# Kernel optimization log

Hardware: AMD Instinct MI355X
Metric: run time of the kernel (lower is better)

## Reference

```python
import jax, jax.numpy as jnp
import numpy as np


def setup_inputs() -> dict:
    key = jax.random.key(0)
    ks = jax.random.split(key, 8)
    B, C, H, W = 4, 256, 64, 64
    Cqk = C // 8
    s = 1.0 / np.sqrt(C)
    return {
        "x": jax.random.normal(ks[0], (B, C, H, W), jnp.float32),
        "wq": jax.random.normal(ks[1], (Cqk, C), jnp.float32) * s,
        "bq": jax.random.normal(ks[2], (Cqk,), jnp.float32) * 0.01,
        "wk": jax.random.normal(ks[3], (Cqk, C), jnp.float32) * s,
        "bk": jax.random.normal(ks[4], (Cqk,), jnp.float32) * 0.01,
        "wv": jax.random.normal(ks[5], (C, C), jnp.float32) * s,
        "bv": jax.random.normal(ks[6], (C,), jnp.float32) * 0.01,
        "gamma": jax.random.normal(ks[7], (1,), jnp.float32),
    }


def reference(x, wq, bq, wk, bk, wv, bv, gamma):
    B, C, H, W = x.shape
    N = H * W
    xf = x.reshape(B, C, N)  # [B, C, N]
    # 1x1 convs are per-pixel channel matmuls
    q = jnp.einsum('oc,bcn->bon', wq, xf) + bq[None, :, None]  # [B, C//8, N]
    k = jnp.einsum('oc,bcn->bon', wk, xf) + bk[None, :, None]  # [B, C//8, N]
    v = jnp.einsum('oc,bcn->bon', wv, xf) + bv[None, :, None]  # [B, C, N]
    # energy[b, n, m] = q[b,:,n] . k[b,:,m]  (unscaled)
    energy = jnp.einsum('bcn,bcm->bnm', q, k)  # [B, N, N]
    # original applies softmax over dim=-2, i.e. over the query index n per column m
    attn = jax.nn.softmax(energy, axis=-2)  # [B, N, N]
    at_map = jnp.transpose(attn, (0, 2, 1))  # returned map, [B, N, N]
    # sa_map = V @ attn : bmm([B,C,N],[B,N,N]) -> [B,C,N]
    sa = jnp.einsum('bcn,bnm->bcm', v, attn).reshape(B, C, H, W)
    out = x + gamma[0] * sa
    return (out, at_map)
```

## Files before the change

### kernel.cpp

```cpp
#include <hip/hip_runtime.h>
#include <hip/hip_bf16.h>
#include <cstdint>
#include <cstddef>

#define NPIX 4096
#define CIN  256
#define CQK  32
#define BSZ  4

typedef __attribute__((ext_vector_type(8))) short          bf16x8;
typedef __attribute__((ext_vector_type(4))) float          f32x4;
typedef __attribute__((ext_vector_type(8))) unsigned short u16x8;

static __device__ inline unsigned short f2bf(float f) {
    __hip_bfloat16 h = __float2bfloat16(f);
    unsigned short u;
    __builtin_memcpy(&u, &h, 2);
    return u;
}

static __device__ inline void gl2lds16(const void* g, void* l) {
    __builtin_amdgcn_global_load_lds(
        (const __attribute__((address_space(1))) unsigned int*)g,
        (__attribute__((address_space(3))) unsigned int*)l,
        16, 0, 0);
}

__global__ __launch_bounds__(256) void proj_kernel(
    const float* __restrict__ x, const float* __restrict__ W,
    const float* __restrict__ bias, float* __restrict__ y, int Cout)
{
    __shared__ float Wl[8][CIN];
    const int t  = threadIdx.x;
    const int n0 = blockIdx.x * 1024;
    const int o0 = blockIdx.y * 8;
    const int b  = blockIdx.z;

    #pragma unroll
    for (int j = 0; j < 8; ++j) {
        int flat = t + 256 * j;
        int row = flat >> 8, col = flat & 255;
        Wl[row][col] = W[(o0 + row) * CIN + col];
    }
    __syncthreads();

    float acc[8][4];
    #pragma unroll
    for (int o = 0; o < 8; ++o)
        #pragma unroll
        for (int i = 0; i < 4; ++i) acc[o][i] = 0.f;

    const float* xb = x + ((size_t)b * CIN) * NPIX + n0 + t * 4;
    #pragma unroll 4
    for (int c = 0; c < CIN; ++c) {
        float4 xv = *(const float4*)(xb + (size_t)c * NPIX);
        #pragma unroll
        for (int o = 0; o < 8; ++o) {
            float w = Wl[o][c];
            acc[o][0] = fmaf(w, xv.x, acc[o][0]);
            acc[o][1] = fmaf(w, xv.y, acc[o][1]);
            acc[o][2] = fmaf(w, xv.z, acc[o][2]);
            acc[o][3] = fmaf(w, xv.w, acc[o][3]);
        }
    }
    #pragma unroll
    for (int o = 0; o < 8; ++o) {
        float bb = bias[o0 + o];
        float4 r = { acc[o][0] + bb, acc[o][1] + bb,
                     acc[o][2] + bb, acc[o][3] + bb };
        *(float4*)(y + ((size_t)(b * Cout + o0 + o)) * NPIX + n0 + t * 4) = r;
    }
}

__global__ __launch_bounds__(256) void proj_qk_kernel(
    const float* __restrict__ x,
    const float* __restrict__ wq, const float* __restrict__ bq,
    const float* __restrict__ wk, const float* __restrict__ bk,
    float* __restrict__ qout, float* __restrict__ kout)
{
    __shared__ float Wl[CIN][12];
    const int t  = threadIdx.x;
    const int n0 = blockIdx.x * 512;
    const int og = blockIdx.y * 8;
    const int b  = blockIdx.z;
    const bool isK = og >= CQK;
    const float* W    = isK ? wk : wq;
    const float* bias = isK ? bk : bq;
    float* y          = isK ? kout : qout;
    const int o0      = isK ? og - CQK : og;

    #pragma unroll
    for (int j = 0; j < 8; ++j) {
        int flat = t + 256 * j;
        int o = flat >> 8, c = flat & 255;
        Wl[c][o] = W[(o0 + o) * CIN + c];
    }
    __syncthreads();

    float acc[8][2];
    #pragma unroll
    for (int o = 0; o < 8; ++o) { acc[o][0] = 0.f; acc[o][1] = 0.f; }

    const float* xb = x + ((size_t)b * CIN) * NPIX + n0 + t * 2;
    #pragma unroll 4
    for (int c = 0; c < CIN; ++c) {
        float2 xv = *(const float2*)(xb + (size_t)c * NPIX);
        f32x4 w0 = *(const f32x4*)&Wl[c][0];
        f32x4 w1 = *(const f32x4*)&Wl[c][4];
        float wv[8] = { w0[0], w0[1], w0[2], w0[3],
                        w1[0], w1[1], w1[2], w1[3] };
        #pragma unroll
        for (int o = 0; o < 8; ++o) {
            acc[o][0] = fmaf(wv[o], xv.x, acc[o][0]);
            acc[o][1] = fmaf(wv[o], xv.y, acc[o][1]);
        }
    }
    #pragma unroll
    for (int o = 0; o < 8; ++o) {
        float bb = bias[o0 + o];
        float2 r = { acc[o][0] + bb, acc[o][1] + bb };
        *(float2*)(y + ((size_t)(b * CQK + o0 + o)) * NPIX + n0 + t * 2) = r;
    }
}

__global__ __launch_bounds__(256) void proj_v_bf16_kernel(
    const float* __restrict__ x, const float* __restrict__ W,
    const float* __restrict__ bias, unsigned short* __restrict__ y)
{
    __shared__ float Wl[CIN][20];
    const int t  = threadIdx.x;
    const int n0 = blockIdx.x * 512;
    const int o0 = blockIdx.y * 16;
    const int b  = blockIdx.z;

    #pragma unroll
    for (int j = 0; j < 16; ++j) {
        int flat = t + 256 * j;
        int o = flat >> 8, c = flat & 255;
        Wl[c][o] = W[(o0 + o) * CIN + c];
    }
    __syncthreads();

    float acc[16][2];
    #pragma unroll
    for (int o = 0; o < 16; ++o) { acc[o][0] = 0.f; acc[o][1] = 0.f; }

    const float* xb = x + ((size_t)b * CIN) * NPIX + n0 + t * 2;
    #pragma unroll 2
    for (int c = 0; c < CIN; ++c) {
        float2 xv = *(const float2*)(xb + (size_t)c * NPIX);
        f32x4 w0 = *(const f32x4*)&Wl[c][0];
        f32x4 w1 = *(const f32x4*)&Wl[c][4];
        f32x4 w2 = *(const f32x4*)&Wl[c][8];
        f32x4 w3 = *(const f32x4*)&Wl[c][12];
        float wv[16] = { w0[0], w0[1], w0[2], w0[3],
                         w1[0], w1[1], w1[2], w1[3],
                         w2[0], w2[1], w2[2], w2[3],
                         w3[0], w3[1], w3[2], w3[3] };
        #pragma unroll
        for (int o = 0; o < 16; ++o) {
            acc[o][0] = fmaf(wv[o], xv.x, acc[o][0]);
            acc[o][1] = fmaf(wv[o], xv.y, acc[o][1]);
        }
    }
    #pragma unroll
    for (int o = 0; o < 16; ++o) {
        float bb = bias[o0 + o];
        ushort2 r;
        r.x = f2bf(acc[o][0] + bb);
        r.y = f2bf(acc[o][1] + bb);
        *(ushort2*)(y + ((size_t)(b * CIN + o0 + o)) * NPIX + n0 + t * 2) = r;
    }
}

__global__ __launch_bounds__(512) void energy_softmax_kernel(
    const float* __restrict__ q, const float* __restrict__ k,
    float* __restrict__ at_map, unsigned short* __restrict__ attn_bf,
    float* __restrict__ inv_buf)
{
    __shared__ float kk[CQK][12];
    __shared__ float wredM[8][8];
    __shared__ float wredS[8][8];
    const int t  = threadIdx.x;
    const int m0 = blockIdx.x * 8;
    const int b  = blockIdx.y;
    const int lane = t & 63, wid = t >> 6;

    if (t < 256) {
        int c = t >> 3, mi = t & 7;
        kk[c][mi] = k[((size_t)(b * CQK + c)) * NPIX + m0 + mi];
    }
    __syncthreads();

    float s[8][8];
    #pragma unroll
    for (int mi = 0; mi < 8; ++mi)
        #pragma unroll
        for (int i = 0; i < 8; ++i) s[mi][i] = 0.f;

    const float* qb = q + ((size_t)b * CQK) * NPIX + t * 8;
    #pragma unroll 2
    for (int c = 0; c < CQK; ++c) {
        float4 q0 = *(const float4*)(qb + (size_t)c * NPIX);
        float4 q1 = *(const float4*)(qb + (size_t)c * NPIX + 4);
        f32x4 k0 = *(const f32x4*)&kk[c][0];
        f32x4 k1 = *(const f32x4*)&kk[c][4];
        float kv[8] = { k0[0], k0[1], k0[2], k0[3],
                        k1[0], k1[1], k1[2], k1[3] };
        #pragma unroll
        for (int mi = 0; mi < 8; ++mi) {
            float w = kv[mi];
            s[mi][0] = fmaf(w, q0.x, s[mi][0]);
            s[mi][1] = fmaf(w, q0.y, s[mi][1]);
            s[mi][2] = fmaf(w, q0.z, s[mi][2]);
            s[mi][3] = fmaf(w, q0.w, s[mi][3]);
            s[mi][4] = fmaf(w, q1.x, s[mi][4]);
            s[mi][5] = fmaf(w, q1.y, s[mi][5]);
            s[mi][6] = fmaf(w, q1.z, s[mi][6]);
            s[mi][7] = fmaf(w, q1.w, s[mi][7]);
        }
    }

    #pragma unroll
    for (int mi = 0; mi < 8; ++mi) {
        float mx = s[mi][0];
        #pragma unroll
        for (int i = 1; i < 8; ++i) mx = fmaxf(mx, s[mi][i]);
        #pragma unroll
        for (int off = 1; off < 64; off <<= 1)
            mx = fmaxf(mx, __shfl_xor(mx, off, 64));
        if (lane == 0) wredM[mi][wid] = mx;
    }
    __syncthreads();

    #pragma unroll
    for (int mi = 0; mi < 8; ++mi) {
        float bmx = wredM[mi][0];
        #pragma unroll
        for (int w = 1; w < 8; ++w) bmx = fmaxf(bmx, wredM[mi][w]);
        float sum = 0.f;
        #pragma unroll
        for (int i = 0; i < 8; ++i) {
            s[mi][i] = __expf(s[mi][i] - bmx);
            sum += s[mi][i];
        }
        if (attn_bf) {
            size_t rowoff = ((size_t)(b * NPIX) + m0 + mi) * NPIX + t * 8;
            u16x8 rb;
            #pragma unroll
            for (int i = 0; i < 8; ++i) rb[i] = f2bf(s[mi][i]);
            *(u16x8*)(attn_bf + rowoff) = rb;
        }
        #pragma unroll
        for (int off = 1; off < 64; off <<= 1)
            sum += __shfl_xor(sum, off, 64);
        if (lane == 0) wredS[mi][wid] = sum;
    }
    __syncthreads();

    #pragma unroll
    for (int mi = 0; mi < 8; ++mi) {
        float bsum = 0.f;
        #pragma unroll
        for (int w = 0; w < 8; ++w) bsum += wredS[mi][w];
        float inv = 1.f / bsum;
        if (inv_buf && t == mi) inv_buf[(size_t)b * NPIX + m0 + mi] = inv;
        size_t rowoff = ((size_t)(b * NPIX) + m0 + mi) * NPIX + t * 8;
        float4 r0 = { s[mi][0]*inv, s[mi][1]*inv, s[mi][2]*inv, s[mi][3]*inv };
        float4 r1 = { s[mi][4]*inv, s[mi][5]*inv, s[mi][6]*inv, s[mi][7]*inv };
        *(float4*)(at_map + rowoff)     = r0;
        *(float4*)(at_map + rowoff + 4) = r1;
    }
}

__global__ __launch_bounds__(256) void sa_gemm_mfma(
    const unsigned short* __restrict__ v,
    const unsigned short* __restrict__ attn,
    const float* __restrict__ x, const float* __restrict__ gptr,
    const float* __restrict__ inv_buf,
    float* __restrict__ out)
{
    __shared__ __align__(16) unsigned short As[128 * 64];
    __shared__ __align__(16) unsigned short Bs[64 * 64];

    const int t = threadIdx.x, lane = t & 63, w = t >> 6;

    const int gid  = blockIdx.x;
    const int xcd  = gid & 7;
    const int slot = gid >> 3;
    const int c_t     = slot & 1;
    const int m_local = (slot >> 1) & 7;
    const int b       = slot >> 4;
    const int m_base = (xcd * 8 + m_local) * 64;
    const int c_base = c_t * 128;
    const int wc = (w >> 1) * 64, wm = (w & 1) * 32;

    const int lrow = lane >> 3;
    const int glog = (lane & 7) ^ lrow;
    const unsigned short* aSrc[4];
    const unsigned short* bSrc[2];
    #pragma unroll
    for (int qi = 0; qi < 4; ++qi)
        aSrc[qi] = v    + ((size_t)(b * CIN + c_base + w * 32 + qi * 8 + lrow)) * NPIX + glog * 8;
    #pragma unroll
    for (int qi = 0; qi < 2; ++qi)
        bSrc[qi] = attn + ((size_t)b * NPIX + m_base + w * 16 + qi * 8 + lrow) * NPIX + glog * 8;

    const int l15 = lane & 15, q4 = lane >> 4;
    const int x0 = (q4 ^ (lane & 7)) * 8;
    const int x1 = ((q4 ^ 4) ^ (lane & 7)) * 8;
    const int baseA = (wc + l15) * 64;
    const int baseB = (wm + l15) * 64;

    f32x4 acc[4][2];
    #pragma unroll
    for (int i = 0; i < 4; ++i)
        #pragma unroll
        for (int j = 0; j < 2; ++j) acc[i][j] = (f32x4)(0.0f);

    for (int k0 = 0; k0 < NPIX; k0 += 64) {
        #pragma unroll
        for (int qi = 0; qi < 4; ++qi)
            gl2lds16(aSrc[qi] + k0, &As[(w * 32 + qi * 8) * 64]);
        #pragma unroll
        for (int qi = 0; qi < 2; ++qi)
            gl2lds16(bSrc[qi] + k0, &Bs[(w * 16 + qi * 8) * 64]);
        __syncthreads();
        #pragma unroll
        for (int ks = 0; ks < 2; ++ks) {
            const int xo = ks ? x1 : x0;
            bf16x8 af[4], bfr[2];
            #pragma unroll
            for (int i = 0; i < 4; ++i)
                af[i] = *(const bf16x8*)&As[baseA + i * 1024 + xo];
            #pragma unroll
            for (int j = 0; j < 2; ++j)
                bfr[j] = *(const bf16x8*)&Bs[baseB + j * 1024 + xo];
            #pragma unroll
            for (int i = 0; i < 4; ++i)
                #pragma unroll
                for (int j = 0; j < 2; ++j)
                    acc[i][j] = __builtin_amdgcn_mfma_f32_16x16x32_bf16(
                        af[i], bfr[j], acc[i][j], 0, 0, 0);
        }
        __syncthreads();
    }

    const float g = gptr[0];
    float invm[2];
    #pragma unroll
    for (int j = 0; j < 2; ++j)
        invm[j] = inv_buf[(size_t)b * NPIX + m_base + wm + j * 16 + l15];
    #pragma unroll
    for (int i = 0; i < 4; ++i) {
        int c = c_base + wc + i * 16 + q4 * 4;
        #pragma unroll
        for (int j = 0; j < 2; ++j) {
            int m = m_base + wm + j * 16 + l15;
            float gi = g * invm[j];
            #pragma unroll
            for (int r = 0; r < 4; ++r) {
                size_t idx = ((size_t)(b * CIN + c + r)) * NPIX + m;
                out[idx] = x[idx] + gi * acc[i][j][r];
            }
        }
    }
}

__global__ __launch_bounds__(256) void sa_gemm_kernel(
    const float* __restrict__ v, const float* __restrict__ at_map,
    const float* __restrict__ x, const float* __restrict__ gptr,
    float* __restrict__ out)
{
    __shared__ float Vt[32][68];
    __shared__ float At[32][68];
    const int t  = threadIdx.x;
    const int m0 = blockIdx.x * 64;
    const int c0 = blockIdx.y * 64;
    const int b  = blockIdx.z;
    const int r  = t >> 2, qd = t & 3;
    const int tc = t & 15, tm = t >> 4;

    const float* vb = v      + ((size_t)(b * CIN  + c0 + r)) * NPIX + qd * 4;
    const float* ab = at_map + ((size_t)(b * NPIX + m0 + r)) * NPIX + qd * 4;

    float acc[4][4];
    #pragma unroll
    for (int i = 0; i < 4; ++i)
        #pragma unroll
        for (int j = 0; j < 4; ++j) acc[i][j] = 0.f;

    for (int n0 = 0; n0 < NPIX; n0 += 32) {
        float4 v0 = *(const float4*)(vb + n0);
        float4 v1 = *(const float4*)(vb + n0 + 16);
        float4 a0 = *(const float4*)(ab + n0);
        float4 a1 = *(const float4*)(ab + n0 + 16);
        Vt[qd*4+0][r] = v0.x; Vt[qd*4+1][r] = v0.y;
        Vt[qd*4+2][r] = v0.z; Vt[qd*4+3][r] = v0.w;
        Vt[16+qd*4+0][r] = v1.x; Vt[16+qd*4+1][r] = v1.y;
        Vt[16+qd*4+2][r] = v1.z; Vt[16+qd*4+3][r] = v1.w;
        At[qd*4+0][r] = a0.x; At[qd*4+1][r] = a0.y;
        At[qd*4+2][r] = a0.z; At[qd*4+3][r] = a0.w;
        At[16+qd*4+0][r] = a1.x; At[16+qd*4+1][r] = a1.y;
        At[16+qd*4+2][r] = a1.z; At[16+qd*4+3][r] = a1.w;
        __syncthreads();
        #pragma unroll
        for (int kk = 0; kk < 32; ++kk) {
            float4 a  = *(const float4*)&Vt[kk][tc * 4];
            float4 bb = *(const float4*)&At[kk][tm * 4];
            acc[0][0] = fmaf(a.x, bb.x, acc[0][0]);
            acc[0][1] = fmaf(a.x, bb.y, acc[0][1]);
            acc[0][2] = fmaf(a.x, bb.z, acc[0][2]);
            acc[0][3] = fmaf(a.x, bb.w, acc[0][3]);
            acc[1][0] = fmaf(a.y, bb.x, acc[1][0]);
            acc[1][1] = fmaf(a.y, bb.y, acc[1][1]);
            acc[1][2] = fmaf(a.y, bb.z, acc[1][2]);
            acc[1][3] = fmaf(a.y, bb.w, acc[1][3]);
            acc[2][0] = fmaf(a.z, bb.x, acc[2][0]);
            acc[2][1] = fmaf(a.z, bb.y, acc[2][1]);
            acc[2][2] = fmaf(a.z, bb.z, acc[2][2]);
            acc[2][3] = fmaf(a.z, bb.w, acc[2][3]);
            acc[3][0] = fmaf(a.w, bb.x, acc[3][0]);
            acc[3][1] = fmaf(a.w, bb.y, acc[3][1]);
            acc[3][2] = fmaf(a.w, bb.z, acc[3][2]);
            acc[3][3] = fmaf(a.w, bb.w, acc[3][3]);
        }
        __syncthreads();
    }

    const float g = *gptr;
    #pragma unroll
    for (int i = 0; i < 4; ++i) {
        size_t row = ((size_t)(b * CIN + c0 + tc * 4 + i)) * NPIX + m0 + tm * 4;
        float4 xv = *(const float4*)(x + row);
        float4 o  = { xv.x + g * acc[i][0], xv.y + g * acc[i][1],
                      xv.z + g * acc[i][2], xv.w + g * acc[i][3] };
        *(float4*)(out + row) = o;
    }
}

extern "C" void kernel_launch(void* const* d_in, const int* in_sizes, int n_in,
                              void* d_out, int out_size, void* d_ws, size_t ws_size,
                              hipStream_t stream) {
    const float* x     = (const float*)d_in[0];
    const float* wq    = (const float*)d_in[1];
    const float* bq    = (const float*)d_in[2];
    const float* wk    = (const float*)d_in[3];
    const float* bk    = (const float*)d_in[4];
    const float* wv    = (const float*)d_in[5];
    const float* bv    = (const float*)d_in[6];
    const float* gamma = (const float*)d_in[7];

    float* out    = (float*)d_out;
    float* at_map = out + (size_t)BSZ * CIN * NPIX;

    const size_t qk_elems  = (size_t)BSZ * CQK * NPIX;
    const size_t v_elems   = (size_t)BSZ * CIN * NPIX;
    const size_t nn_elems  = (size_t)BSZ * NPIX * NPIX;
    const size_t inv_elems = (size_t)BSZ * NPIX;

    const size_t need_fast = 2 * qk_elems * 4 + v_elems * 2 + nn_elems * 2
                           + inv_elems * 4;

    if (ws_size >= need_fast) {
        float*          q       = (float*)d_ws;
        float*          k       = q + qk_elems;
        unsigned short* v_bf    = (unsigned short*)(k + qk_elems);
        unsigned short* attn_bf = v_bf + v_elems;
        float*          inv_buf = (float*)(attn_bf + nn_elems);

        proj_qk_kernel<<<dim3(NPIX/512, 8, BSZ), 256, 0, stream>>>(
            x, wq, bq, wk, bk, q, k);
        proj_v_bf16_kernel<<<dim3(NPIX/512, CIN/16, BSZ), 256, 0, stream>>>(
            x, wv, bv, v_bf);

        energy_softmax_kernel<<<dim3(NPIX/8, BSZ), 512, 0, stream>>>(
            q, k, at_map, attn_bf, inv_buf);

        sa_gemm_mfma<<<dim3(512, 1, 1), 256, 0, stream>>>(
            v_bf, attn_bf, x, gamma, inv_buf, out);
    } else {
        float* q = (float*)d_ws;
        float* k = q + qk_elems;
        float* v = k + qk_elems;

        proj_kernel<<<dim3(NPIX/1024, CQK/8, BSZ), 256, 0, stream>>>(x, wq, bq, q, CQK);
        proj_kernel<<<dim3(NPIX/1024, CQK/8, BSZ), 256, 0, stream>>>(x, wk, bk, k, CQK);
        proj_kernel<<<dim3(NPIX/1024, CIN/8, BSZ), 256, 0, stream>>>(x, wv, bv, v, CIN);

        energy_softmax_kernel<<<dim3(NPIX/8, BSZ), 512, 0, stream>>>(
            q, k, at_map, nullptr, nullptr);

        sa_gemm_kernel<<<dim3(NPIX/64, CIN/64, BSZ), 256, 0, stream>>>(
            v, at_map, x, gamma, out);
    }
}
```

Baseline: 539.7 us.

## Fuse energy, softmax and attention-value GEMM into one two-pass flash-style kernel

Replaces the separate energy/softmax kernel and the bf16 attention GEMM with a single kernel. Each block makes two passes over the keys: the first computes column-wise online max and sum, the second recomputes energies, writes the normalized fp32 attention map and feeds bf16 probabilities through LDS into MFMA against V. This drops the bf16 NxN intermediate buffer write and read and one kernel launch. In exchange it recomputes the QK dot products twice, and each block now covers all 256 channels, which changes occupancy and LDS usage.

Result: no change. 544.4 us (+0.9%).

```diff
diff --git a/kernel.cpp b/kernel.cpp
--- a/kernel.cpp
+++ b/kernel.cpp
@@ -7,6 +7,8 @@
 #define CIN  256
 #define CQK  32
 #define BSZ  4
+#define MT   32
+#define NT   64
 
 typedef __attribute__((ext_vector_type(8))) short          bf16x8;
 typedef __attribute__((ext_vector_type(4))) float          f32x4;
@@ -175,8 +177,7 @@
 
 __global__ __launch_bounds__(512) void energy_softmax_kernel(
     const float* __restrict__ q, const float* __restrict__ k,
-    float* __restrict__ at_map, unsigned short* __restrict__ attn_bf,
-    float* __restrict__ inv_buf)
+    float* __restrict__ at_map)
 {
     __shared__ float kk[CQK][12];
     __shared__ float wredM[8][8];
@@ -244,13 +245,6 @@
             s[mi][i] = __expf(s[mi][i] - bmx);
             sum += s[mi][i];
         }
-        if (attn_bf) {
-            size_t rowoff = ((size_t)(b * NPIX) + m0 + mi) * NPIX + t * 8;
-            u16x8 rb;
-            #pragma unroll
-            for (int i = 0; i < 8; ++i) rb[i] = f2bf(s[mi][i]);
-            *(u16x8*)(attn_bf + rowoff) = rb;
-        }
         #pragma unroll
         for (int off = 1; off < 64; off <<= 1)
             sum += __shfl_xor(sum, off, 64);
@@ -264,7 +258,6 @@
         #pragma unroll
         for (int w = 0; w < 8; ++w) bsum += wredS[mi][w];
         float inv = 1.f / bsum;
-        if (inv_buf && t == mi) inv_buf[(size_t)b * NPIX + m0 + mi] = inv;
         size_t rowoff = ((size_t)(b * NPIX) + m0 + mi) * NPIX + t * 8;
         float4 r0 = { s[mi][0]*inv, s[mi][1]*inv, s[mi][2]*inv, s[mi][3]*inv };
         float4 r1 = { s[mi][4]*inv, s[mi][5]*inv, s[mi][6]*inv, s[mi][7]*inv };
@@ -273,44 +266,114 @@
     }
 }
 
-__global__ __launch_bounds__(256) void sa_gemm_mfma(
+__global__ __launch_bounds__(256) void fused_attn_kernel(
+    const float* __restrict__ q,
+    const float* __restrict__ k,
     const unsigned short* __restrict__ v,
-    const unsigned short* __restrict__ attn,
     const float* __restrict__ x, const float* __restrict__ gptr,
-    const float* __restrict__ inv_buf,
-    float* __restrict__ out)
+    float* __restrict__ at_map, float* __restrict__ out)
 {
-    __shared__ __align__(16) unsigned short As[128 * 64];
-    __shared__ __align__(16) unsigned short Bs[64 * 64];
+    __shared__ __align__(16) unsigned short Vs[CIN * NT];
+    __shared__ __align__(16) float          Qs[2][CQK * NT];
+    __shared__ __align__(16) unsigned short Ps[MT * 72];
+    __shared__ float Ks[CQK][MT];
+    __shared__ float MaxS[MT], InvS[MT];
 
     const int t = threadIdx.x, lane = t & 63, w = t >> 6;
 
-    const int gid  = blockIdx.x;
-    const int xcd  = gid & 7;
-    const int slot = gid >> 3;
-    const int c_t     = slot & 1;
-    const int m_local = (slot >> 1) & 7;
-    const int b       = slot >> 4;
-    const int m_base = (xcd * 8 + m_local) * 64;
-    const int c_base = c_t * 128;
-    const int wc = (w >> 1) * 64, wm = (w & 1) * 32;
-
+    const int gid = blockIdx.x;
+    const int xcd = gid & 7, slot = gid >> 3;
+    const int b = xcd & 3;
+    const int m0 = (slot + ((xcd >> 2) << 6)) * MT;
+
+    const int nq = lane & 15;
+    const int mp = w * 4 + (lane >> 4);
+    const int mA = 2 * mp, mB = 2 * mp + 1;
+    const int l15 = lane & 15, q4 = lane >> 4;
+    const int wc = w * 64;
+    const int xo0 = (q4 ^ (l15 & 7)) * 8;
+    const int xo1 = ((q4 ^ 4) ^ (l15 & 7)) * 8;
     const int lrow = lane >> 3;
     const int glog = (lane & 7) ^ lrow;
-    const unsigned short* aSrc[4];
-    const unsigned short* bSrc[2];
-    #pragma unroll
-    for (int qi = 0; qi < 4; ++qi)
-        aSrc[qi] = v    + ((size_t)(b * CIN + c_base + w * 32 + qi * 8 + lrow)) * NPIX + glog * 8;
-    #pragma unroll
-    for (int qi = 0; qi < 2; ++qi)
-        bSrc[qi] = attn + ((size_t)b * NPIX + m_base + w * 16 + qi * 8 + lrow) * NPIX + glog * 8;
-
-    const int l15 = lane & 15, q4 = lane >> 4;
-    const int x0 = (q4 ^ (lane & 7)) * 8;
-    const int x1 = ((q4 ^ 4) ^ (lane & 7)) * 8;
-    const int baseA = (wc + l15) * 64;
-    const int baseB = (wm + l15) * 64;
+
+    const float* qbase = q + (size_t)b * CQK * NPIX;
+    const unsigned short* vbase = v + (size_t)b * CIN * NPIX;
+
+    for (int i = t; i < CQK * MT; i += 256) {
+        int c = i >> 5, m = i & 31;
+        Ks[c][m] = k[((size_t)(b * CQK + c)) * NPIX + m0 + m];
+    }
+    #pragma unroll
+    for (int jj = 0; jj < 2; ++jj) {
+        int c0 = w * 8 + jj * 4;
+        gl2lds16(qbase + (size_t)(c0 + (lane >> 4)) * NPIX + (lane & 15) * 4,
+                 &Qs[0][c0 * NT]);
+    }
+    __syncthreads();
+
+    float M0 = -1e30f, M1 = -1e30f, S0 = 0.f, S1 = 0.f;
+
+    for (int tile = 0; tile < NPIX / NT; ++tile) {
+        const int cur = tile & 1;
+        if (tile + 1 < NPIX / NT) {
+            #pragma unroll
+            for (int jj = 0; jj < 2; ++jj) {
+                int c0 = w * 8 + jj * 4;
+                gl2lds16(qbase + (size_t)(c0 + (lane >> 4)) * NPIX
+                               + (tile + 1) * NT + (lane & 15) * 4,
+                         &Qs[cur ^ 1][c0 * NT]);
+            }
+        }
+        float sA[4] = {0.f,0.f,0.f,0.f}, sB[4] = {0.f,0.f,0.f,0.f};
+        #pragma unroll 8
+        for (int c = 0; c < CQK; ++c) {
+            f32x4 qv = *(const f32x4*)&Qs[cur][c * NT + nq * 4];
+            float2 kv = *(const float2*)&Ks[c][mA];
+            #pragma unroll
+            for (int i = 0; i < 4; ++i) {
+                sA[i] = fmaf(kv.x, qv[i], sA[i]);
+                sB[i] = fmaf(kv.y, qv[i], sB[i]);
+            }
+        }
+        float tA = fmaxf(fmaxf(sA[0], sA[1]), fmaxf(sA[2], sA[3]));
+        float tB = fmaxf(fmaxf(sB[0], sB[1]), fmaxf(sB[2], sB[3]));
+        if (tA > M0) { S0 *= __expf(M0 - tA); M0 = tA; }
+        if (tB > M1) { S1 *= __expf(M1 - tB); M1 = tB; }
+        #pragma unroll
+        for (int i = 0; i < 4; ++i) {
+            S0 += __expf(sA[i] - M0);
+            S1 += __expf(sB[i] - M1);
+        }
+        __syncthreads();
+    }
+
+    #pragma unroll
+    for (int off = 1; off < 16; off <<= 1) {
+        float Mo = __shfl_xor(M0, off, 16);
+        float So = __shfl_xor(S0, off, 16);
+        float Mn = fmaxf(M0, Mo);
+        S0 = S0 * __expf(M0 - Mn) + So * __expf(Mo - Mn);
+        M0 = Mn;
+        Mo = __shfl_xor(M1, off, 16);
+        So = __shfl_xor(S1, off, 16);
+        Mn = fmaxf(M1, Mo);
+        S1 = S1 * __expf(M1 - Mn) + So * __expf(Mo - Mn);
+        M1 = Mn;
+    }
+    if ((lane & 15) == 0) {
+        MaxS[mA] = M0; InvS[mA] = 1.f / S0;
+        MaxS[mB] = M1; InvS[mB] = 1.f / S1;
+    }
+    #pragma unroll
+    for (int jj = 0; jj < 2; ++jj) {
+        int c0 = w * 8 + jj * 4;
+        gl2lds16(qbase + (size_t)(c0 + (lane >> 4)) * NPIX + (lane & 15) * 4,
+                 &Qs[0][c0 * NT]);
+    }
+    __syncthreads();
+
+    const float Mh0 = MaxS[mA], Mh1 = MaxS[mB];
+    const float I0  = InvS[mA], I1  = InvS[mB];
 
     f32x4 acc[4][2];
     #pragma unroll
@@ -318,24 +381,65 @@
         #pragma unroll
         for (int j = 0; j < 2; ++j) acc[i][j] = (f32x4)(0.0f);
 
-    for (int k0 = 0; k0 < NPIX; k0 += 64) {
-        #pragma unroll
-        for (int qi = 0; qi < 4; ++qi)
-            gl2lds16(aSrc[qi] + k0, &As[(w * 32 + qi * 8) * 64]);
-        #pragma unroll
-        for (int qi = 0; qi < 2; ++qi)
-            gl2lds16(bSrc[qi] + k0, &Bs[(w * 16 + qi * 8) * 64]);
+    for (int tile = 0; tile < NPIX / NT; ++tile) {
+        const int cur = tile & 1;
+        #pragma unroll
+        for (int qi = 0; qi < 8; ++qi)
+            gl2lds16(vbase + (size_t)(w * 64 + qi * 8 + lrow) * NPIX
+                           + tile * NT + glog * 8,
+                     &Vs[(w * 64 + qi * 8) * NT]);
+        if (tile + 1 < NPIX / NT) {
+            #pragma unroll
+            for (int jj = 0; jj < 2; ++jj) {
+                int c0 = w * 8 + jj * 4;
+                gl2lds16(qbase + (size_t)(c0 + (lane >> 4)) * NPIX
+                               + (tile + 1) * NT + (lane & 15) * 4,
+                         &Qs[cur ^ 1][c0 * NT]);
+            }
+        }
+        float sA[4] = {0.f,0.f,0.f,0.f}, sB[4] = {0.f,0.f,0.f,0.f};
+        #pragma unroll 8
+        for (int c = 0; c < CQK; ++c) {
+            f32x4 qv = *(const f32x4*)&Qs[cur][c * NT + nq * 4];
+            float2 kv = *(const float2*)&Ks[c][mA];
+            #pragma unroll
+            for (int i = 0; i < 4; ++i) {
+                sA[i] = fmaf(kv.x, qv[i], sA[i]);
+                sB[i] = fmaf(kv.y, qv[i], sB[i]);
+            }
+        }
+        float pA[4], pB[4];
+        #pragma unroll
+        for (int i = 0; i < 4; ++i) {
+            pA[i] = __expf(sA[i] - Mh0);
+            pB[i] = __expf(sB[i] - Mh1);
+        }
+        {
+            size_t rowA = ((size_t)(b * NPIX) + m0 + mA) * NPIX + tile * NT + nq * 4;
+            size_t rowB = ((size_t)(b * NPIX) + m0 + mB) * NPIX + tile * NT + nq * 4;
+            f32x4 wA = { pA[0]*I0, pA[1]*I0, pA[2]*I0, pA[3]*I0 };
+            f32x4 wB = { pB[0]*I1, pB[1]*I1, pB[2]*I1, pB[3]*I1 };
+            *(f32x4*)(at_map + rowA) = wA;
+            *(f32x4*)(at_map + rowB) = wB;
+        }
+        {
+            ushort4 ua, ub;
+            ua.x = f2bf(pA[0]); ua.y = f2bf(pA[1]); ua.z = f2bf(pA[2]); ua.w = f2bf(pA[3]);
+            ub.x = f2bf(pB[0]); ub.y = f2bf(pB[1]); ub.z = f2bf(pB[2]); ub.w = f2bf(pB[3]);
+            *(ushort4*)&Ps[mA * 72 + nq * 4] = ua;
+            *(ushort4*)&Ps[mB * 72 + nq * 4] = ub;
+        }
         __syncthreads();
         #pragma unroll
         for (int ks = 0; ks < 2; ++ks) {
-            const int xo = ks ? x1 : x0;
+            const int xo = ks ? xo1 : xo0;
             bf16x8 af[4], bfr[2];
             #pragma unroll
             for (int i = 0; i < 4; ++i)
-                af[i] = *(const bf16x8*)&As[baseA + i * 1024 + xo];
+                af[i] = *(const bf16x8*)&Vs[(wc + i * 16 + l15) * NT + xo];
             #pragma unroll
             for (int j = 0; j < 2; ++j)
-                bfr[j] = *(const bf16x8*)&Bs[baseB + j * 1024 + xo];
+                bfr[j] = *(const bf16x8*)&Ps[(j * 16 + l15) * 72 + ks * 32 + q4 * 8];
             #pragma unroll
             for (int i = 0; i < 4; ++i)
                 #pragma unroll
@@ -347,16 +451,13 @@
     }
 
     const float g = gptr[0];
-    float invm[2];
-    #pragma unroll
-    for (int j = 0; j < 2; ++j)
-        invm[j] = inv_buf[(size_t)b * NPIX + m_base + wm + j * 16 + l15];
+    float invm[2] = { InvS[l15], InvS[16 + l15] };
     #pragma unroll
     for (int i = 0; i < 4; ++i) {
-        int c = c_base + wc + i * 16 + q4 * 4;
+        int c = wc + i * 16 + q4 * 4;
         #pragma unroll
         for (int j = 0; j < 2; ++j) {
-            int m = m_base + wm + j * 16 + l15;
+            int m = m0 + j * 16 + l15;
             float gi = g * invm[j];
             #pragma unroll
             for (int r = 0; r < 4; ++r) {
@@ -456,29 +557,21 @@
 
     const size_t qk_elems  = (size_t)BSZ * CQK * NPIX;
     const size_t v_elems   = (size_t)BSZ * CIN * NPIX;
-    const size_t nn_elems  = (size_t)BSZ * NPIX * NPIX;
-    const size_t inv_elems = (size_t)BSZ * NPIX;
-
-    const size_t need_fast = 2 * qk_elems * 4 + v_elems * 2 + nn_elems * 2
-                           + inv_elems * 4;
+
+    const size_t need_fast = 2 * qk_elems * 4 + v_elems * 2;
 
     if (ws_size >= need_fast) {
-        float*          q       = (float*)d_ws;
-        float*          k       = q + qk_elems;
-        unsigned short* v_bf    = (unsigned short*)(k + qk_elems);
-        unsigned short* attn_bf = v_bf + v_elems;
-        float*          inv_buf = (float*)(attn_bf + nn_elems);
+        float*          q    = (float*)d_ws;
+        float*          k    = q + qk_elems;
+        unsigned short* v_bf = (unsigned short*)(k + qk_elems);
 
         proj_qk_kernel<<<dim3(NPIX/512, 8, BSZ), 256, 0, stream>>>(
             x, wq, bq, wk, bk, q, k);
         proj_v_bf16_kernel<<<dim3(NPIX/512, CIN/16, BSZ), 256, 0, stream>>>(
             x, wv, bv, v_bf);
 
-        energy_softmax_kernel<<<dim3(NPIX/8, BSZ), 512, 0, stream>>>(
-            q, k, at_map, attn_bf, inv_buf);
-
-        sa_gemm_mfma<<<dim3(512, 1, 1), 256, 0, stream>>>(
-            v_bf, attn_bf, x, gamma, inv_buf, out);
+        fused_attn_kernel<<<dim3(512, 1, 1), 256, 0, stream>>>(
+            q, k, v_bf, x, gamma, at_map, out);
     } else {
         float* q = (float*)d_ws;
         float* k = q + qk_elems;
@@ -488,8 +581,7 @@
         proj_kernel<<<dim3(NPIX/1024, CQK/8, BSZ), 256, 0, stream>>>(x, wk, bk, k, CQK);
         proj_kernel<<<dim3(NPIX/1024, CIN/8, BSZ), 256, 0, stream>>>(x, wv, bv, v, CIN);
 
-        energy_softmax_kernel<<<dim3(NPIX/8, BSZ), 512, 0, stream>>>(
-            q, k, at_map, nullptr, nullptr);
+        energy_softmax_kernel<<<dim3(NPIX/8, BSZ), 512, 0, stream>>>(q, k, at_map);
 
         sa_gemm_kernel<<<dim3(NPIX/64, CIN/64, BSZ), 256, 0, stream>>>(
             v, at_map, x, gamma, out);
```
